# Performance work log

Measured on AMD Instinct MI355X. Metric: run time of the kernel, lower is better.

## Reference

```python
import jax, jax.numpy as jnp
from jax import lax
import numpy as np

T, B, HIDDEN, MLPW, DATA = 256, 4096, 64, 128, 8
TSCALE = 1.0

def lipswish(x):
    return 0.909 * jax.nn.silu(x)

def setup_inputs() -> dict:
    key = jax.random.key(0)
    ks = jax.random.split(key, 8)
    def lin(k, i, o):
        return jax.random.normal(k, (i, o), jnp.float32) / np.float32(np.sqrt(i))
    inp = dict(
        ts=jnp.linspace(0.0, 1.0, T, dtype=jnp.float32),
        batch_size=B,
        dW=jax.random.normal(ks[0], (T - 1, B, HIDDEN), jnp.float32),
        drift_W0=lin(ks[1], 1 + HIDDEN, MLPW), drift_b0=jnp.zeros((MLPW,), jnp.float32),
        drift_W1=lin(ks[2], MLPW, MLPW),       drift_b1=jnp.zeros((MLPW,), jnp.float32),
        drift_Wo=lin(ks[3], MLPW, HIDDEN),     drift_bo=jnp.zeros((HIDDEN,), jnp.float32),
        diff_W0=lin(ks[4], 1 + HIDDEN, MLPW),  diff_b0=jnp.zeros((MLPW,), jnp.float32),
        diff_W1=lin(ks[5], MLPW, MLPW),        diff_b1=jnp.zeros((MLPW,), jnp.float32),
        diff_Wo=lin(ks[6], MLPW, HIDDEN),      diff_bo=jnp.zeros((HIDDEN,), jnp.float32),
        readout_W=lin(ks[7], HIDDEN, DATA),    readout_b=jnp.zeros((DATA,), jnp.float32),
    )
    return inp

def reference(ts, batch_size, dW,
              drift_W0, drift_b0, drift_W1, drift_b1, drift_Wo, drift_bo,
              diff_W0, diff_b0, diff_W1, diff_b1, diff_Wo, diff_bo,
              readout_W, readout_b):
    dt = ts[1] - ts[0]  # uniform grid, dt_scale = 1.0

    def mlp(tx, W0, b0, W1, b1, Wo, bo):
        h = lipswish(tx @ W0 + b0)
        h = lipswish(h @ W1 + b1)
        return TSCALE * jnp.tanh(h @ Wo + bo)  # tanh-clamped output

    def f_and_g(t, x):
        tcol = t * jnp.ones((x.shape[0], 1), x.dtype)
        tx = jnp.concatenate([tcol, x], axis=1)  # (B, 1+H)
        f = mlp(tx, drift_W0, drift_b0, drift_W1, drift_b1, drift_Wo, drift_bo)
        g = mlp(tx, diff_W0, diff_b0, diff_W1, diff_b1, diff_Wo, diff_bo)  # diagonal noise
        return f, g

    x0 = jnp.ones((batch_size, HIDDEN), jnp.float32)  # fixed initial point
    f0, g0 = f_and_g(ts[0], x0)
    dWs = dW * jnp.sqrt(dt)  # Brownian increments N(0, dt)

    # Reversible Heun (Stratonovich):
    #   zhat_{n+1} = 2 z_n - zhat_n + f(t_n, zhat_n) dt + g(t_n, zhat_n) dW_n
    #   z_{n+1}    = z_n + 0.5 (f_n + f_{n+1}) dt + 0.5 (g_n + g_{n+1}) dW_n
    def step(carry, inp):
        z, zhat, f, g = carry
        t_next, dw = inp
        zhat_n = 2.0 * z - zhat + f * dt + g * dw
        f_n, g_n = f_and_g(t_next, zhat_n)
        z_n = z + 0.5 * (f + f_n) * dt + 0.5 * (g + g_n) * dw
        return (z_n, zhat_n, f_n, g_n), z_n

    _, zs = lax.scan(step, (x0, x0, f0, g0), (ts[1:], dWs))
    xs = jnp.concatenate([x0[None], zs], axis=0)  # (T, B, H)
    ys = jnp.einsum('tbh,hd->tbd', xs, readout_W) + readout_b  # (T, B, D)
    ys = ys.transpose(1, 0, 2)  # (B, T, D)
    ts_e = jnp.broadcast_to(ts[None, :, None], (batch_size, ts.shape[0], 1))
    # linear_interpolation_coeffs on NaN-free data returns the values unchanged
    return jnp.concatenate([ts_e, ys], axis=2)  # (B, T, 1+D)
```

## Files before the change

### kernel.cpp

```cpp
#include <hip/hip_runtime.h>
#include <math.h>

#define T_STEPS 256
#define BATCH   4096
#define HID     64
#define MW      128
#define DOUT    8
#define RPB     16
#define NTH     512
#define NW      8
#define AS      72
#define HS      136

typedef _Float16 half8 __attribute__((ext_vector_type(8)));
typedef float    f32x4 __attribute__((ext_vector_type(4)));

__device__ __forceinline__ float fast_rcp(float x) { return __builtin_amdgcn_rcpf(x); }
__device__ __forceinline__ float lipswish(float x) {
    float e = __expf(-x);
    return 0.909f * x * fast_rcp(1.0f + e);
}
__device__ __forceinline__ float fast_tanh(float x) {
    float e = __expf(2.0f * x);
    return 1.0f - 2.0f * fast_rcp(e + 1.0f);
}

#define MFMA(a, b, c) __builtin_amdgcn_mfma_f32_16x16x32_f16((a), (b), (c), 0, 0, 0)


__global__ __launch_bounds__(NTH, 2)
void sde_kernel(const float* __restrict__ ts,
                const float* __restrict__ dW,
                const float* __restrict__ dW0, const float* __restrict__ db0,
                const float* __restrict__ dW1, const float* __restrict__ db1,
                const float* __restrict__ dWo, const float* __restrict__ dbo,
                const float* __restrict__ gW0, const float* __restrict__ gb0,
                const float* __restrict__ gW1, const float* __restrict__ gb1,
                const float* __restrict__ gWo, const float* __restrict__ gbo,
                const float* __restrict__ rW,  const float* __restrict__ rb,
                float* __restrict__ out)
{
    __shared__ _Float16 Ain_hi[RPB][AS];
    __shared__ _Float16 Ain_lo[RPB][AS];
    __shared__ _Float16 h1b[2][RPB][HS];
    __shared__ _Float16 h2b[2][RPB][HS];
    __shared__ _Float16 zb[2][RPB][AS];
    __shared__ _Float16 fgb[2][RPB][HID];
    __shared__ float    bias1t[2 * MW];
    __shared__ float    tsS[T_STEPS];

    const int tid  = threadIdx.x;
    const int lane = tid & 63;
    const int wid  = tid >> 6;
    const int l15  = lane & 15;
    const int quad = lane >> 4;
    const int mlp  = wid >> 2;
    const int nq   = wid & 3;
    const int rowbase = blockIdx.x * RPB;

    for (int i = tid; i < T_STEPS; i += NTH) tsS[i] = ts[i];

    const float t0   = ts[0];
    const float dt   = ts[1] - t0;
    const float sqdt = sqrtf(dt);

    const float* W0 = mlp ? gW0 : dW0;
    const float* W1 = mlp ? gW1 : dW1;
    const float* Wo = mlp ? gWo : dWo;

    half8 bw1[2][2], bw2[4][2], bw3[4];
    #pragma unroll
    for (int kt = 0; kt < 2; ++kt)
        #pragma unroll
        for (int nt = 0; nt < 2; ++nt) {
            half8 v;
            #pragma unroll
            for (int j = 0; j < 8; ++j) {
                const int k = kt * 32 + quad * 8 + j;
                const int n = nq * 32 + nt * 16 + l15;
                v[j] = (_Float16)W0[(1 + k) * MW + n];
            }
            bw1[kt][nt] = v;
        }
    #pragma unroll
    for (int kt = 0; kt < 4; ++kt)
        #pragma unroll
        for (int nt = 0; nt < 2; ++nt) {
            half8 v;
            #pragma unroll
            for (int j = 0; j < 8; ++j) {
                const int k = kt * 32 + quad * 8 + j;
                const int n = nq * 32 + nt * 16 + l15;
                v[j] = (_Float16)W1[k * MW + n];
            }
            bw2[kt][nt] = v;
        }
    #pragma unroll
    for (int kt = 0; kt < 4; ++kt) {
        half8 v;
        #pragma unroll
        for (int j = 0; j < 8; ++j) {
            const int k = kt * 32 + quad * 8 + j;
            const int n = nq * 16 + l15;
            v[j] = (_Float16)Wo[k * HID + n];
        }
        bw3[kt] = v;
    }

    float b2v[2], b3v;
    {
        const float* b1p = mlp ? gb1 : db1;
        const float* bop = mlp ? gbo : dbo;
        #pragma unroll
        for (int nt = 0; nt < 2; ++nt) b2v[nt] = b1p[nq * 32 + nt * 16 + l15];
        b3v = bop[nq * 16 + l15];
    }

    half8 brd[2];
    float rbv = 0.0f;
    int   ocol = 0;
    if (wid == 0) {
        #pragma unroll
        for (int kt = 0; kt < 2; ++kt) {
            half8 v;
            #pragma unroll
            for (int j = 0; j < 8; ++j) {
                const int k = kt * 32 + quad * 8 + j;
                v[j] = (l15 < 8) ? (_Float16)rW[k * DOUT + l15] : (_Float16)0.0f;
            }
            brd[kt] = v;
        }
        rbv  = (l15 < 8) ? rb[l15] : 0.0f;
        ocol = (l15 == 8) ? 0 : (l15 + 1);
    }

    float b0s = 0.0f, w0s = 0.0f;
    if (tid < 2 * MW) {
        b0s = (tid < MW ? db0 : gb0)[tid & (MW - 1)];
        w0s = (tid < MW ? dW0 : gW0)[tid & (MW - 1)];
    }

    const int ud = lane;
    float z[2], zh[2], fold[2], gold[2], dwr[2], dn[2];
    #pragma unroll
    for (int i = 0; i < 2; ++i) { z[i] = 1.0f; zh[i] = 1.0f; dwr[i] = 0.0f; }

    #pragma unroll
    for (int i = 0; i < 2; ++i) {
        const int r = wid + NW * i;
        Ain_hi[r][ud] = (_Float16)1.0f;
        Ain_lo[r][ud] = (_Float16)0.0f;
        dn[i] = dW[(size_t)(rowbase + r) * HID + ud];
    }
    if (tid < 2 * MW) bias1t[tid] = b0s + t0 * w0s;
    __syncthreads();

    for (int n = 1; n <= T_STEPS; ++n) {
        {
            const int koff = quad * 8;
            half8 ah[2], al[2];
            #pragma unroll
            for (int kt = 0; kt < 2; ++kt) {
                ah[kt] = *(const half8*)&Ain_hi[l15][kt * 32 + koff];
                al[kt] = *(const half8*)&Ain_lo[l15][kt * 32 + koff];
            }
            f32x4 acc[2];
            #pragma unroll
            for (int nt = 0; nt < 2; ++nt) {
                const float b = bias1t[mlp * MW + nq * 32 + nt * 16 + l15];
                acc[nt] = (f32x4){b, b, b, b};
            }
            #pragma unroll
            for (int nt = 0; nt < 2; ++nt)
                #pragma unroll
                for (int kt = 0; kt < 2; ++kt) {
                    acc[nt] = MFMA(ah[kt], bw1[kt][nt], acc[nt]);
                    acc[nt] = MFMA(al[kt], bw1[kt][nt], acc[nt]);
                }
            #pragma unroll
            for (int nt = 0; nt < 2; ++nt)
                #pragma unroll
                for (int i2 = 0; i2 < 4; ++i2) {
                    const float v = lipswish(acc[nt][i2]);
                    h1b[mlp][quad * 4 + i2][nq * 32 + nt * 16 + l15] = (_Float16)v;
                }

            if (wid == 0 && n >= 2) {
                const int q = (n - 1) & 1, s = n - 2;
                half8 a0 = *(const half8*)&zb[q][l15][koff];
                half8 a1 = *(const half8*)&zb[q][l15][32 + koff];
                f32x4 racc = (f32x4){rbv, rbv, rbv, rbv};
                racc = MFMA(a0, brd[0], racc);
                racc = MFMA(a1, brd[1], racc);
                if (l15 < 9) {
                    const float tv = tsS[s];
                    #pragma unroll
                    for (int i2 = 0; i2 < 4; ++i2) {
                        const int r = quad * 4 + i2;
                        out[(size_t)(rowbase + r) * (T_STEPS * 9) + s * 9 + ocol]
                            = (l15 < 8) ? racc[i2] : tv;
                    }
                }
            }
        }
        __syncthreads();

        {
            half8 a[4];
            #pragma unroll
            for (int kt = 0; kt < 4; ++kt)
                a[kt] = *(const half8*)&h1b[mlp][l15][kt * 32 + quad * 8];
            f32x4 acc[2];
            #pragma unroll
            for (int nt = 0; nt < 2; ++nt)
                acc[nt] = (f32x4){b2v[nt], b2v[nt], b2v[nt], b2v[nt]};
            #pragma unroll
            for (int nt = 0; nt < 2; ++nt)
                #pragma unroll
                for (int kt = 0; kt < 4; ++kt)
                    acc[nt] = MFMA(a[kt], bw2[kt][nt], acc[nt]);
            #pragma unroll
            for (int nt = 0; nt < 2; ++nt)
                #pragma unroll
                for (int i2 = 0; i2 < 4; ++i2) {
                    const float v = lipswish(acc[nt][i2]);
                    h2b[mlp][quad * 4 + i2][nq * 32 + nt * 16 + l15] = (_Float16)v;
                }
        }
        __syncthreads();

        {
            half8 a[4];
            #pragma unroll
            for (int kt = 0; kt < 4; ++kt)
                a[kt] = *(const half8*)&h2b[mlp][l15][kt * 32 + quad * 8];
            f32x4 acc = (f32x4){b3v, b3v, b3v, b3v};
            #pragma unroll
            for (int kt = 0; kt < 4; ++kt)
                acc = MFMA(a[kt], bw3[kt], acc);
            #pragma unroll
            for (int i2 = 0; i2 < 4; ++i2)
                fgb[mlp][quad * 4 + i2][nq * 16 + l15]
                    = (_Float16)fast_tanh(acc[i2]);
        }
        __syncthreads();

        {
            float fn[2], gn[2];
            #pragma unroll
            for (int i = 0; i < 2; ++i) {
                const int r = wid + NW * i;
                fn[i] = (float)fgb[0][r][ud];
                gn[i] = (float)fgb[1][r][ud];
            }
            if (n > 1) {
                #pragma unroll
                for (int i = 0; i < 2; ++i)
                    z[i] += 0.5f * (fold[i] + fn[i]) * dt + 0.5f * (gold[i] + gn[i]) * dwr[i];
            }
            const int p = n & 1;
            #pragma unroll
            for (int i = 0; i < 2; ++i)
                zb[p][wid + NW * i][ud] = (_Float16)z[i];

            if (n < T_STEPS) {
                const int np = (n < T_STEPS - 2) ? n : (T_STEPS - 2);
                #pragma unroll
                for (int i = 0; i < 2; ++i) {
                    const int r = wid + NW * i;
                    dwr[i] = dn[i] * sqdt;
                    dn[i]  = dW[(size_t)np * (BATCH * HID) + (size_t)(rowbase + r) * HID + ud];
                    zh[i]  = 2.0f * z[i] - zh[i] + fn[i] * dt + gn[i] * dwr[i];
                    const _Float16 hi = (_Float16)zh[i];
                    Ain_hi[r][ud] = hi;
                    Ain_lo[r][ud] = (_Float16)(zh[i] - (float)hi);
                }
                if (tid < 2 * MW) bias1t[tid] = b0s + tsS[n] * w0s;
            }
            #pragma unroll
            for (int i = 0; i < 2; ++i) { fold[i] = fn[i]; gold[i] = gn[i]; }
        }
        __syncthreads();
    }

    if (wid == 0) {
        const int koff = quad * 8, s = T_STEPS - 1;
        half8 a0 = *(const half8*)&zb[0][l15][koff];
        half8 a1 = *(const half8*)&zb[0][l15][32 + koff];
        f32x4 racc = (f32x4){rbv, rbv, rbv, rbv};
        racc = MFMA(a0, brd[0], racc);
        racc = MFMA(a1, brd[1], racc);
        if (l15 < 9) {
            const float tv = tsS[s];
            #pragma unroll
            for (int i2 = 0; i2 < 4; ++i2) {
                const int r = quad * 4 + i2;
                out[(size_t)(rowbase + r) * (T_STEPS * 9) + s * 9 + ocol]
                    = (l15 < 8) ? racc[i2] : tv;
            }
        }
    }
}

extern "C" void kernel_launch(void* const* d_in, const int* in_sizes, int n_in,
                              void* d_out, int out_size, void* d_ws, size_t ws_size,
                              hipStream_t stream) {
    const float* ts  = (const float*)d_in[0];
    const float* dW  = (const float*)d_in[2];
    const float* dW0 = (const float*)d_in[3];
    const float* db0 = (const float*)d_in[4];
    const float* dW1 = (const float*)d_in[5];
    const float* db1 = (const float*)d_in[6];
    const float* dWo = (const float*)d_in[7];
    const float* dbo = (const float*)d_in[8];
    const float* gW0 = (const float*)d_in[9];
    const float* gb0 = (const float*)d_in[10];
    const float* gW1 = (const float*)d_in[11];
    const float* gb1 = (const float*)d_in[12];
    const float* gWo = (const float*)d_in[13];
    const float* gbo = (const float*)d_in[14];
    const float* rW  = (const float*)d_in[15];
    const float* rb  = (const float*)d_in[16];
    float* out = (float*)d_out;

    sde_kernel<<<dim3(BATCH / RPB), dim3(NTH), 0, stream>>>(
        ts, dW, dW0, db0, dW1, db1, dWo, dbo,
        gW0, gb0, gW1, gb1, gWo, gbo, rW, rb, out);
}
```

Before: 714.1 us.

## Halve rows per block to launch more blocks, padding MFMA tiles with zeros

Each block now integrates 8 batch rows instead of 16, which doubles the grid to 512 blocks and raises the launch-bounds occupancy target to 4 blocks per CU. The MFMA tiles keep 16 rows, with the upper 8 zero-padded and their outputs masked on store. The aim is to spread the serial 256-step recurrence over more CUs and hide latency with more resident blocks. In exchange, half of every MFMA's work is wasted and weight loads and barriers are repeated per block. The tighter register budget may also cause spills.

```diff
diff --git a/kernel.cpp b/kernel.cpp
--- a/kernel.cpp
+++ b/kernel.cpp
@@ -6,7 +6,8 @@
 #define HID     64
 #define MW      128
 #define DOUT    8
-#define RPB     16
+#define RPB     8
+#define MROWS   16
 #define NTH     512
 #define NW      8
 #define AS      72
@@ -28,7 +29,7 @@
 #define MFMA(a, b, c) __builtin_amdgcn_mfma_f32_16x16x32_f16((a), (b), (c), 0, 0, 0)
 
 
-__global__ __launch_bounds__(NTH, 2)
+__global__ __launch_bounds__(NTH, 4)
 void sde_kernel(const float* __restrict__ ts,
                 const float* __restrict__ dW,
                 const float* __restrict__ dW0, const float* __restrict__ db0,
@@ -40,12 +41,12 @@
                 const float* __restrict__ rW,  const float* __restrict__ rb,
                 float* __restrict__ out)
 {
-    __shared__ _Float16 Ain_hi[RPB][AS];
-    __shared__ _Float16 Ain_lo[RPB][AS];
-    __shared__ _Float16 h1b[2][RPB][HS];
-    __shared__ _Float16 h2b[2][RPB][HS];
-    __shared__ _Float16 zb[2][RPB][AS];
-    __shared__ _Float16 fgb[2][RPB][HID];
+    __shared__ _Float16 Ain_hi[MROWS][AS];
+    __shared__ _Float16 Ain_lo[MROWS][AS];
+    __shared__ _Float16 h1b[2][MROWS][HS];
+    __shared__ _Float16 h2b[2][MROWS][HS];
+    __shared__ _Float16 zb[2][MROWS][AS];
+    __shared__ _Float16 fgb[2][MROWS][HID];
     __shared__ float    bias1t[2 * MW];
     __shared__ float    tsS[T_STEPS];
 
@@ -141,17 +142,17 @@
     }
 
     const int ud = lane;
-    float z[2], zh[2], fold[2], gold[2], dwr[2], dn[2];
-    #pragma unroll
-    for (int i = 0; i < 2; ++i) { z[i] = 1.0f; zh[i] = 1.0f; dwr[i] = 0.0f; }
-
-    #pragma unroll
-    for (int i = 0; i < 2; ++i) {
-        const int r = wid + NW * i;
-        Ain_hi[r][ud] = (_Float16)1.0f;
-        Ain_lo[r][ud] = (_Float16)0.0f;
-        dn[i] = dW[(size_t)(rowbase + r) * HID + ud];
-    }
+    float z = 1.0f, zh = 1.0f, fold, gold, dwr = 0.0f, dn;
+
+    Ain_hi[wid][ud] = (_Float16)1.0f;
+    Ain_lo[wid][ud] = (_Float16)0.0f;
+    Ain_hi[wid + RPB][ud] = (_Float16)0.0f;
+    Ain_lo[wid + RPB][ud] = (_Float16)0.0f;
+    zb[0][wid][ud] = (_Float16)0.0f;
+    zb[1][wid][ud] = (_Float16)0.0f;
+    zb[0][wid + RPB][ud] = (_Float16)0.0f;
+    zb[1][wid + RPB][ud] = (_Float16)0.0f;
+    dn = dW[(size_t)(rowbase + wid) * HID + ud];
     if (tid < 2 * MW) bias1t[tid] = b0s + t0 * w0s;
     __syncthreads();
 
@@ -192,7 +193,7 @@
                 f32x4 racc = (f32x4){rbv, rbv, rbv, rbv};
                 racc = MFMA(a0, brd[0], racc);
                 racc = MFMA(a1, brd[1], racc);
-                if (l15 < 9) {
+                if (l15 < 9 && quad < RPB / 4) {
                     const float tv = tsS[s];
                     #pragma unroll
                     for (int i2 = 0; i2 < 4; ++i2) {
@@ -246,39 +247,24 @@
         __syncthreads();
 
         {
-            float fn[2], gn[2];
-            #pragma unroll
-            for (int i = 0; i < 2; ++i) {
-                const int r = wid + NW * i;
-                fn[i] = (float)fgb[0][r][ud];
-                gn[i] = (float)fgb[1][r][ud];
-            }
-            if (n > 1) {
-                #pragma unroll
-                for (int i = 0; i < 2; ++i)
-                    z[i] += 0.5f * (fold[i] + fn[i]) * dt + 0.5f * (gold[i] + gn[i]) * dwr[i];
-            }
+            const float fn = (float)fgb[0][wid][ud];
+            const float gn = (float)fgb[1][wid][ud];
+            if (n > 1)
+                z += 0.5f * (fold + fn) * dt + 0.5f * (gold + gn) * dwr;
             const int p = n & 1;
-            #pragma unroll
-            for (int i = 0; i < 2; ++i)
-                zb[p][wid + NW * i][ud] = (_Float16)z[i];
+            zb[p][wid][ud] = (_Float16)z;
 
             if (n < T_STEPS) {
                 const int np = (n < T_STEPS - 2) ? n : (T_STEPS - 2);
-                #pragma unroll
-                for (int i = 0; i < 2; ++i) {
-                    const int r = wid + NW * i;
-                    dwr[i] = dn[i] * sqdt;
-                    dn[i]  = dW[(size_t)np * (BATCH * HID) + (size_t)(rowbase + r) * HID + ud];
-                    zh[i]  = 2.0f * z[i] - zh[i] + fn[i] * dt + gn[i] * dwr[i];
-                    const _Float16 hi = (_Float16)zh[i];
-                    Ain_hi[r][ud] = hi;
-                    Ain_lo[r][ud] = (_Float16)(zh[i] - (float)hi);
-                }
+                dwr = dn * sqdt;
+                dn  = dW[(size_t)np * (BATCH * HID) + (size_t)(rowbase + wid) * HID + ud];
+                zh  = 2.0f * z - zh + fn * dt + gn * dwr;
+                const _Float16 hi = (_Float16)zh;
+                Ain_hi[wid][ud] = hi;
+                Ain_lo[wid][ud] = (_Float16)(zh - (float)hi);
                 if (tid < 2 * MW) bias1t[tid] = b0s + tsS[n] * w0s;
             }
-            #pragma unroll
-            for (int i = 0; i < 2; ++i) { fold[i] = fn[i]; gold[i] = gn[i]; }
+            fold = fn; gold = gn;
         }
         __syncthreads();
     }
@@ -290,7 +276,7 @@
         f32x4 racc = (f32x4){rbv, rbv, rbv, rbv};
         racc = MFMA(a0, brd[0], racc);
         racc = MFMA(a1, brd[1], racc);
-        if (l15 < 9) {
+        if (l15 < 9 && quad < RPB / 4) {
             const float tv = tsS[s];
             #pragma unroll
             for (int i2 = 0; i2 < 4; ++i2) {
```

After: 1.090 ms. +52.7%, slower.

## Fuse output layer with SDE update to drop a barrier and fgb staging

Applied to the files above, without the earlier changes.

Waves 0-3 now run both the drift and diffusion output-layer MFMAs and apply the tanh and the reversible Heun update directly from registers. This removes the fgb shared buffer and one __syncthreads per step, and f and g stay in fp32 instead of being rounded to half. Waves 4-7 take over the readout store and the time-bias update in parallel. Half the waves now idle during the last stage, and launch bounds drop to one block per CU to make room for the extra registers, which may cut occupancy.

```diff
diff --git a/kernel.cpp b/kernel.cpp
--- a/kernel.cpp
+++ b/kernel.cpp
@@ -8,7 +8,6 @@
 #define DOUT    8
 #define RPB     16
 #define NTH     512
-#define NW      8
 #define AS      72
 #define HS      136
 
@@ -28,7 +27,7 @@
 #define MFMA(a, b, c) __builtin_amdgcn_mfma_f32_16x16x32_f16((a), (b), (c), 0, 0, 0)
 
 
-__global__ __launch_bounds__(NTH, 2)
+__global__ __launch_bounds__(NTH, 1)
 void sde_kernel(const float* __restrict__ ts,
                 const float* __restrict__ dW,
                 const float* __restrict__ dW0, const float* __restrict__ db0,
@@ -45,7 +44,6 @@
     __shared__ _Float16 h1b[2][RPB][HS];
     __shared__ _Float16 h2b[2][RPB][HS];
     __shared__ _Float16 zb[2][RPB][AS];
-    __shared__ _Float16 fgb[2][RPB][HID];
     __shared__ float    bias1t[2 * MW];
     __shared__ float    tsS[T_STEPS];
 
@@ -66,9 +64,8 @@
 
     const float* W0 = mlp ? gW0 : dW0;
     const float* W1 = mlp ? gW1 : dW1;
-    const float* Wo = mlp ? gWo : dWo;
-
-    half8 bw1[2][2], bw2[4][2], bw3[4];
+
+    half8 bw1[2][2], bw2[4][2];
     #pragma unroll
     for (int kt = 0; kt < 2; ++kt)
         #pragma unroll
@@ -95,31 +92,48 @@
             }
             bw2[kt][nt] = v;
         }
-    #pragma unroll
-    for (int kt = 0; kt < 4; ++kt) {
-        half8 v;
-        #pragma unroll
-        for (int j = 0; j < 8; ++j) {
-            const int k = kt * 32 + quad * 8 + j;
-            const int n = nq * 16 + l15;
-            v[j] = (_Float16)Wo[k * HID + n];
-        }
-        bw3[kt] = v;
-    }
-
-    float b2v[2], b3v;
+
+    float b2v[2];
     {
         const float* b1p = mlp ? gb1 : db1;
-        const float* bop = mlp ? gbo : dbo;
         #pragma unroll
         for (int nt = 0; nt < 2; ++nt) b2v[nt] = b1p[nq * 32 + nt * 16 + l15];
-        b3v = bop[nq * 16 + l15];
+    }
+
+    const int ucol = nq * 16 + l15;
+    const int urow = quad * 4;
+
+    half8 bw3f[4], bw3g[4];
+    float b3f = 0.0f, b3g = 0.0f;
+    float z[4], zh[4], fold[4], gold[4], dwr[4], dn[4];
+    if (wid < 4) {
+        #pragma unroll
+        for (int kt = 0; kt < 4; ++kt) {
+            half8 vf, vg;
+            #pragma unroll
+            for (int j = 0; j < 8; ++j) {
+                const int k = kt * 32 + quad * 8 + j;
+                vf[j] = (_Float16)dWo[k * HID + ucol];
+                vg[j] = (_Float16)gWo[k * HID + ucol];
+            }
+            bw3f[kt] = vf;
+            bw3g[kt] = vg;
+        }
+        b3f = dbo[ucol];
+        b3g = gbo[ucol];
+        #pragma unroll
+        for (int i = 0; i < 4; ++i) {
+            z[i] = 1.0f; zh[i] = 1.0f; dwr[i] = 0.0f;
+            dn[i] = dW[(size_t)(rowbase + urow + i) * HID + ucol];
+            Ain_hi[urow + i][ucol] = (_Float16)1.0f;
+            Ain_lo[urow + i][ucol] = (_Float16)0.0f;
+        }
     }
 
     half8 brd[2];
     float rbv = 0.0f;
     int   ocol = 0;
-    if (wid == 0) {
+    if (wid == 4) {
         #pragma unroll
         for (int kt = 0; kt < 2; ++kt) {
             half8 v;
@@ -135,24 +149,12 @@
     }
 
     float b0s = 0.0f, w0s = 0.0f;
-    if (tid < 2 * MW) {
-        b0s = (tid < MW ? db0 : gb0)[tid & (MW - 1)];
-        w0s = (tid < MW ? dW0 : gW0)[tid & (MW - 1)];
-    }
-
-    const int ud = lane;
-    float z[2], zh[2], fold[2], gold[2], dwr[2], dn[2];
-    #pragma unroll
-    for (int i = 0; i < 2; ++i) { z[i] = 1.0f; zh[i] = 1.0f; dwr[i] = 0.0f; }
-
-    #pragma unroll
-    for (int i = 0; i < 2; ++i) {
-        const int r = wid + NW * i;
-        Ain_hi[r][ud] = (_Float16)1.0f;
-        Ain_lo[r][ud] = (_Float16)0.0f;
-        dn[i] = dW[(size_t)(rowbase + r) * HID + ud];
-    }
-    if (tid < 2 * MW) bias1t[tid] = b0s + t0 * w0s;
+    if (tid >= 256) {
+        const int idx = tid - 256;
+        b0s = (idx < MW ? db0 : gb0)[idx & (MW - 1)];
+        w0s = (idx < MW ? dW0 : gW0)[idx & (MW - 1)];
+        bias1t[idx] = b0s + t0 * w0s;
+    }
     __syncthreads();
 
     for (int n = 1; n <= T_STEPS; ++n) {
@@ -184,9 +186,73 @@
                     const float v = lipswish(acc[nt][i2]);
                     h1b[mlp][quad * 4 + i2][nq * 32 + nt * 16 + l15] = (_Float16)v;
                 }
-
-            if (wid == 0 && n >= 2) {
-                const int q = (n - 1) & 1, s = n - 2;
+        }
+        __syncthreads();
+
+        {
+            half8 a[4];
+            #pragma unroll
+            for (int kt = 0; kt < 4; ++kt)
+                a[kt] = *(const half8*)&h1b[mlp][l15][kt * 32 + quad * 8];
+            f32x4 acc[2];
+            #pragma unroll
+            for (int nt = 0; nt < 2; ++nt)
+                acc[nt] = (f32x4){b2v[nt], b2v[nt], b2v[nt], b2v[nt]};
+            #pragma unroll
+            for (int nt = 0; nt < 2; ++nt)
+                #pragma unroll
+                for (int kt = 0; kt < 4; ++kt)
+                    acc[nt] = MFMA(a[kt], bw2[kt][nt], acc[nt]);
+            #pragma unroll
+            for (int nt = 0; nt < 2; ++nt)
+                #pragma unroll
+                for (int i2 = 0; i2 < 4; ++i2) {
+                    const float v = lipswish(acc[nt][i2]);
+                    h2b[mlp][quad * 4 + i2][nq * 32 + nt * 16 + l15] = (_Float16)v;
+                }
+        }
+        __syncthreads();
+
+        if (wid < 4) {
+            half8 a[4];
+            #pragma unroll
+            for (int kt = 0; kt < 4; ++kt)
+                a[kt] = *(const half8*)&h2b[0][l15][kt * 32 + quad * 8];
+            f32x4 accF = (f32x4){b3f, b3f, b3f, b3f};
+            #pragma unroll
+            for (int kt = 0; kt < 4; ++kt)
+                accF = MFMA(a[kt], bw3f[kt], accF);
+            #pragma unroll
+            for (int kt = 0; kt < 4; ++kt)
+                a[kt] = *(const half8*)&h2b[1][l15][kt * 32 + quad * 8];
+            f32x4 accG = (f32x4){b3g, b3g, b3g, b3g};
+            #pragma unroll
+            for (int kt = 0; kt < 4; ++kt)
+                accG = MFMA(a[kt], bw3g[kt], accG);
+
+            const int p = n & 1;
+            const int np = (n < T_STEPS - 2) ? n : (T_STEPS - 2);
+            #pragma unroll
+            for (int i = 0; i < 4; ++i) {
+                const float fn = fast_tanh(accF[i]);
+                const float gn = fast_tanh(accG[i]);
+                if (n > 1)
+                    z[i] += 0.5f * (fold[i] + fn) * dt + 0.5f * (gold[i] + gn) * dwr[i];
+                zb[p][urow + i][ucol] = (_Float16)z[i];
+                if (n < T_STEPS) {
+                    dwr[i] = dn[i] * sqdt;
+                    dn[i]  = dW[(size_t)np * (BATCH * HID)
+                                + (size_t)(rowbase + urow + i) * HID + ucol];
+                    zh[i]  = 2.0f * z[i] - zh[i] + fn * dt + gn * dwr[i];
+                    const _Float16 hi = (_Float16)zh[i];
+                    Ain_hi[urow + i][ucol] = hi;
+                    Ain_lo[urow + i][ucol] = (_Float16)(zh[i] - (float)hi);
+                }
+                fold[i] = fn; gold[i] = gn;
+            }
+        } else {
+            if (wid == 4 && n >= 2) {
+                const int koff = quad * 8, q = (n - 1) & 1, s = n - 2;
                 half8 a0 = *(const half8*)&zb[q][l15][koff];
                 half8 a1 = *(const half8*)&zb[q][l15][32 + koff];
                 f32x4 racc = (f32x4){rbv, rbv, rbv, rbv};
@@ -202,88 +268,12 @@
                     }
                 }
             }
+            if (n < T_STEPS) bias1t[tid - 256] = b0s + tsS[n] * w0s;
         }
         __syncthreads();
-
-        {
-            half8 a[4];
-            #pragma unroll
-            for (int kt = 0; kt < 4; ++kt)
-                a[kt] = *(const half8*)&h1b[mlp][l15][kt * 32 + quad * 8];
-            f32x4 acc[2];
-            #pragma unroll
-            for (int nt = 0; nt < 2; ++nt)
-                acc[nt] = (f32x4){b2v[nt], b2v[nt], b2v[nt], b2v[nt]};
-            #pragma unroll
-            for (int nt = 0; nt < 2; ++nt)
-                #pragma unroll
-                for (int kt = 0; kt < 4; ++kt)
-                    acc[nt] = MFMA(a[kt], bw2[kt][nt], acc[nt]);
-            #pragma unroll
-            for (int nt = 0; nt < 2; ++nt)
-                #pragma unroll
-                for (int i2 = 0; i2 < 4; ++i2) {
-                    const float v = lipswish(acc[nt][i2]);
-                    h2b[mlp][quad * 4 + i2][nq * 32 + nt * 16 + l15] = (_Float16)v;
-                }
-        }
-        __syncthreads();
-
-        {
-            half8 a[4];
-            #pragma unroll
-            for (int kt = 0; kt < 4; ++kt)
-                a[kt] = *(const half8*)&h2b[mlp][l15][kt * 32 + quad * 8];
-            f32x4 acc = (f32x4){b3v, b3v, b3v, b3v};
-            #pragma unroll
-            for (int kt = 0; kt < 4; ++kt)
-                acc = MFMA(a[kt], bw3[kt], acc);
-            #pragma unroll
-            for (int i2 = 0; i2 < 4; ++i2)
-                fgb[mlp][quad * 4 + i2][nq * 16 + l15]
-                    = (_Float16)fast_tanh(acc[i2]);
-        }
-        __syncthreads();
-
-        {
-            float fn[2], gn[2];
-            #pragma unroll
-            for (int i = 0; i < 2; ++i) {
-                const int r = wid + NW * i;
-                fn[i] = (float)fgb[0][r][ud];
-                gn[i] = (float)fgb[1][r][ud];
-            }
-            if (n > 1) {
-                #pragma unroll
-                for (int i = 0; i < 2; ++i)
-                    z[i] += 0.5f * (fold[i] + fn[i]) * dt + 0.5f * (gold[i] + gn[i]) * dwr[i];
-            }
-            const int p = n & 1;
-            #pragma unroll
-            for (int i = 0; i < 2; ++i)
-                zb[p][wid + NW * i][ud] = (_Float16)z[i];
-
-            if (n < T_STEPS) {
-                const int np = (n < T_STEPS - 2) ? n : (T_STEPS - 2);
-                #pragma unroll
-                for (int i = 0; i < 2; ++i) {
-                    const int r = wid + NW * i;
-                    dwr[i] = dn[i] * sqdt;
-                    dn[i]  = dW[(size_t)np * (BATCH * HID) + (size_t)(rowbase + r) * HID + ud];
-                    zh[i]  = 2.0f * z[i] - zh[i] + fn[i] * dt + gn[i] * dwr[i];
-                    const _Float16 hi = (_Float16)zh[i];
-                    Ain_hi[r][ud] = hi;
-                    Ain_lo[r][ud] = (_Float16)(zh[i] - (float)hi);
-                }
-                if (tid < 2 * MW) bias1t[tid] = b0s + tsS[n] * w0s;
-            }
-            #pragma unroll
-            for (int i = 0; i < 2; ++i) { fold[i] = fn[i]; gold[i] = gn[i]; }
-        }
-        __syncthreads();
-    }
-
-    if (wid == 0) {
+    }
+
+    if (wid == 4) {
         const int koff = quad * 8, s = T_STEPS - 1;
         half8 a0 = *(const half8*)&zb[0][l15][koff];
         half8 a1 = *(const half8*)&zb[0][l15][32 + koff];
```

Result: faster. 681.9 us (-4.5%).
